# Kernel tuning notes

Measured on AMD Instinct MI355X. Metric: run time of the kernel, lower is better.

## Reference

```python
import jax, jax.numpy as jnp
import numpy as np
from jax import lax

_CLIP_MIN = 1e-06
_CLIP_MAX = 1.0
_POS_ALPHA = 0.0005
NUM_CLASSES = 21
RADIUS = 3
HALF_D = RADIUS * RADIUS
POOL = 3
PAD = POOL // 2
IGNORE = 255
LAM = 0.5  # loss_weight_lambda, lambda_way=1


def _max_pool(x):
    # NCHW max pool, kernel=stride=3, padding=1
    return lax.reduce_window(x, -jnp.inf, lax.max,
                             (1, 1, POOL, POOL), (1, 1, POOL, POOL),
                             ((0, 0), (0, 0), (PAD, PAD), (PAD, PAD)))


def _get_pairs(x):
    # stack radius*radius shifted crops -> [N, C, r^2, nh, nw]
    h, w = x.shape[2], x.shape[3]
    nh, nw = h - RADIUS + 1, w - RADIUS + 1
    crops = [x[:, :, y:y + nh, xo:xo + nw] for y in range(RADIUS) for xo in range(RADIUS)]
    return jnp.stack(crops, axis=2)


def _log_det_by_cholesky(m):
    chol = jnp.linalg.cholesky(m)
    return 2.0 * jnp.sum(jnp.log(jnp.diagonal(chol, axis1=-2, axis2=-1) + 1e-08), axis=-1)


def _rmi_lower_bound(labels_4d, probs_4d):
    la = _max_pool(labels_4d)
    pr = _max_pool(probs_4d)
    n, c = la.shape[0], la.shape[1]
    la_v = _get_pairs(la).reshape(n, c, HALF_D, -1)   # [N,C,d,L]
    pr_v = _get_pairs(pr).reshape(n, c, HALF_D, -1)
    la_v = la_v - jnp.mean(la_v, axis=3, keepdims=True)
    pr_v = pr_v - jnp.mean(pr_v, axis=3, keepdims=True)
    la_cov = jnp.einsum('ncdl,ncel->ncde', la_v, la_v)
    pr_cov = jnp.einsum('ncdl,ncel->ncde', pr_v, pr_v)
    eye = jnp.eye(HALF_D, dtype=la_cov.dtype)
    pr_cov_inv = jnp.linalg.inv(pr_cov + eye * _POS_ALPHA)
    la_pr_cov = jnp.einsum('ncdl,ncel->ncde', la_v, pr_v)
    appro_var = la_cov - jnp.einsum('ncde,ncef,ncgf->ncdg', la_pr_cov, pr_cov_inv, la_pr_cov)
    rmi_now = 0.5 * _log_det_by_cholesky(appro_var + eye * _POS_ALPHA)  # [N,C]
    rmi_per_class = jnp.mean(rmi_now.reshape(-1, NUM_CLASSES), axis=0) / float(HALF_D)
    return jnp.sum(rmi_per_class)


def setup_inputs() -> dict:
    key = jax.random.key(0)
    k1, k2 = jax.random.split(key)
    score = jax.random.normal(k1, (4, NUM_CLASSES, 512, 512), dtype=jnp.float32)
    target = jax.random.randint(k2, (4, 512, 512), 0, NUM_CLASSES, dtype=jnp.int64)
    return {"score": score, "target": target}


def reference(score, target):
    # cross entropy with ignore_index=255, mean reduction
    logp = jax.nn.log_softmax(score, axis=1)                      # [N,C,H,W]
    valid_ce = (target != IGNORE)
    safe_t = jnp.where(valid_ce, target, 0)
    nll = -jnp.take_along_axis(logp, safe_t[:, None].astype(jnp.int32), axis=1)[:, 0]
    normal_loss = jnp.sum(jnp.where(valid_ce, nll, 0.0)) / jnp.sum(valid_ce.astype(jnp.float32))

    # valid one-hot labels and masked sigmoid probs
    mask = (target < NUM_CLASSES)                                 # [N,H,W]
    maskf = mask.astype(jnp.float32)
    onehot = jax.nn.one_hot((target * mask).astype(jnp.int32), NUM_CLASSES, dtype=jnp.float32)
    onehot = onehot * maskf[..., None]                            # [N,H,W,C]
    onehot = jnp.transpose(onehot, (0, 3, 1, 2))                  # [N,C,H,W]
    probs = jnp.clip(jax.nn.sigmoid(score) * maskf[:, None], _CLIP_MIN, _CLIP_MAX)

    rmi_loss = _rmi_lower_bound(onehot, probs)
    return LAM * normal_loss + rmi_loss * (1.0 - LAM)
```

## Files before the change

### kernel.cpp

```cpp
#include <hip/hip_runtime.h>
#include <cfloat>
#include <cmath>

#define DEVINL __device__ __forceinline__

constexpr int N_ = 4, C_ = 21, H_ = 512, W_ = 512;
constexpr int P_ = 171;
constexpr int Q_ = 169;
constexpr int NC_ = N_ * C_;
constexpr int HW_ = H_ * W_;
constexpr int PP_ = 29241;
constexpr int PROW_ = 172;
constexpr int PPAD_ = PROW_ * P_;
constexpr int NCOV_ = 189;
constexpr float EPS_ = 5e-4f;
constexpr int RC_ = 29;
constexpr int G_ = 43;

DEVINL constexpr int tstart(int d) { return d * 9 - d * (d - 1) / 2; }

DEVINL float wave_sum(float v) {
#pragma unroll
    for (int o = 32; o > 0; o >>= 1) v += __shfl_down(v, o, 64);
    return v;
}

__global__ __launch_bounds__(256) void k_bits(const int* __restrict__ target,
                                              unsigned* __restrict__ pack) {
    int tid = blockIdx.x * 256 + threadIdx.x;
    if (tid >= N_ * PP_) return;
    int cell = tid % PP_;
    int n = tid / PP_;
    int j = cell % P_;
    int i = cell / P_;
    int hl = 3 * i - 1; if (hl < 0) hl = 0;
    int wl = 3 * j - 1; if (wl < 0) wl = 0;
    int hmax = 3 * i + 1, wmax = 3 * j + 1;
    const int* tb = target + (size_t)n * HW_;
    unsigned oh = 0, px = 0;
#pragma unroll
    for (int r = 0; r < 3; ++r) {
        int hh = hl + r;
        bool hv = hh <= hmax;
        const int* trow = tb + hh * W_;
#pragma unroll
        for (int dc = 0; dc < 3; ++dc) {
            int ww = wl + dc;
            int t = trow[ww];
            if (hv && (ww <= wmax) && t >= 0 && t < C_) {
                oh |= 1u << t;
                px |= 1u << (r * 3 + dc);
            }
        }
    }
    pack[tid] = oh | (px << 23);
}

__global__ __launch_bounds__(256) void k_ce(const float* __restrict__ score,
                                            const int* __restrict__ target,
                                            float* __restrict__ cov_ce) {
    int tid = blockIdx.x * 256 + threadIdx.x;
    int p0 = tid * 4;
    int n = p0 >> 18;
    int hw = p0 & (HW_ - 1);
    const float* sp = score + (size_t)n * C_ * HW_ + hw;

    float4 s[C_];
#pragma unroll
    for (int c = 0; c < C_; ++c)
        s[c] = *(const float4*)(sp + (size_t)c * HW_);
    int4 t4 = *(const int4*)(target + p0);

    float4 se = {0.f, 0.f, 0.f, 0.f};
    float4 stgt = {0.f, 0.f, 0.f, 0.f};
#pragma unroll
    for (int c = 0; c < C_; ++c) {
        se.x += __expf(s[c].x);
        se.y += __expf(s[c].y);
        se.z += __expf(s[c].z);
        se.w += __expf(s[c].w);
        if (t4.x == c) stgt.x = s[c].x;
        if (t4.y == c) stgt.y = s[c].y;
        if (t4.z == c) stgt.z = s[c].z;
        if (t4.w == c) stgt.w = s[c].w;
    }
    float nll = 0.f, cnt = 0.f;
    if (t4.x != 255) { nll += __logf(se.x) - stgt.x; cnt += 1.f; }
    if (t4.y != 255) { nll += __logf(se.y) - stgt.y; cnt += 1.f; }
    if (t4.z != 255) { nll += __logf(se.z) - stgt.z; cnt += 1.f; }
    if (t4.w != 255) { nll += __logf(se.w) - stgt.w; cnt += 1.f; }

    nll = wave_sum(nll);
    cnt = wave_sum(cnt);
    __shared__ float rn[4], rc[4];
    int wv = threadIdx.x >> 6, lane = threadIdx.x & 63;
    if (lane == 0) { rn[wv] = nll; rc[wv] = cnt; }
    __syncthreads();
    if (threadIdx.x == 0) {
        atomicAdd(&cov_ce[NC_ * NCOV_ + 0], rn[0] + rn[1] + rn[2] + rn[3]);
        atomicAdd(&cov_ce[NC_ * NCOV_ + 1], rc[0] + rc[1] + rc[2] + rc[3]);
    }
}

template <int IDX>
DEVINL void do_cell(const float (&f)[3][16], unsigned pk, int c, float* prp, float* lap) {
    unsigned px = pk >> 23;
    float vm = -FLT_MAX;
#pragma unroll
    for (int r = 0; r < 3; ++r)
#pragma unroll
        for (int dc = 0; dc < 3; ++dc)
            vm = fmaxf(vm, ((px >> (r * 3 + dc)) & 1u) ? f[r][IDX + dc] : -FLT_MAX);
    float p = __builtin_amdgcn_rcpf(1.f + __expf(-vm));
    p = fminf(fmaxf(p, 1e-6f), 1.f);
    *prp = p;
    *lap = ((pk >> c) & 1u) ? 1.f : 0.f;
}

__global__ __launch_bounds__(256) void k_pool(const float* __restrict__ score,
                                              const unsigned* __restrict__ pack,
                                              float* __restrict__ pr,
                                              float* __restrict__ la) {
    int tid = blockIdx.x * 256 + threadIdx.x;
    if (tid >= NC_ * P_ * G_) return;
    int g = tid % G_;
    int rest = tid / G_;
    int i = rest % P_;
    int ncidx = rest / P_;
    int n = ncidx / C_;
    int c = ncidx - n * C_;

    int hl = 3 * i - 1; if (hl < 0) hl = 0;
    int b = (g == 0) ? 0 : 12 * g - 4;
    int o3 = (b + 15 < W_) ? 12 : 8;

    const float* sb = score + (size_t)ncidx * HW_ + (size_t)hl * W_ + b;
    float f[3][16];
#pragma unroll
    for (int r = 0; r < 3; ++r) {
        const float* rp = sb + r * W_;
        float4 q0 = *(const float4*)(rp);
        float4 q1 = *(const float4*)(rp + 4);
        float4 q2 = *(const float4*)(rp + 8);
        float4 q3 = *(const float4*)(rp + o3);
        f[r][0] = q0.x;  f[r][1] = q0.y;  f[r][2] = q0.z;  f[r][3] = q0.w;
        f[r][4] = q1.x;  f[r][5] = q1.y;  f[r][6] = q1.z;  f[r][7] = q1.w;
        f[r][8] = q2.x;  f[r][9] = q2.y;  f[r][10] = q2.z; f[r][11] = q2.w;
        f[r][12] = q3.x; f[r][13] = q3.y; f[r][14] = q3.z; f[r][15] = q3.w;
    }

    const unsigned* pkp = pack + n * PP_ + i * P_ + 4 * g;
    size_t ob = (size_t)ncidx * PPAD_ + (size_t)i * PROW_ + 4 * g;
    if (g == 0) {
        do_cell<0>(f, pkp[0], c, pr + ob + 0, la + ob + 0);
        do_cell<2>(f, pkp[1], c, pr + ob + 1, la + ob + 1);
        do_cell<5>(f, pkp[2], c, pr + ob + 2, la + ob + 2);
        do_cell<8>(f, pkp[3], c, pr + ob + 3, la + ob + 3);
    } else {
        do_cell<3>(f, pkp[0], c, pr + ob + 0, la + ob + 0);
        do_cell<6>(f, pkp[1], c, pr + ob + 1, la + ob + 1);
        do_cell<9>(f, pkp[2], c, pr + ob + 2, la + ob + 2);
        if (4 * g + 3 < P_)
            do_cell<12>(f, pkp[3], c, pr + ob + 3, la + ob + 3);
    }
}

template <bool WITH_S1, int D0, int D1>
DEVINL void cov_tri(const float* __restrict__ X, float* __restrict__ cov,
                    int nc, int r0, int rend, int s1base, int s2base,
                    int tid, float (*red)[33]) {
    constexpr int NS2 = ((9 - D0) * (10 - D0) - (9 - D1) * (10 - D1)) / 2;
    constexpr int RLO = D0 / 3;
    constexpr int NS1 = WITH_S1 ? 9 : 0;
    constexpr int KOFF = tstart(D0);
    float s1[9], s2[NS2];
#pragma unroll
    for (int k = 0; k < 9; ++k) s1[k] = 0.f;
#pragma unroll
    for (int k = 0; k < NS2; ++k) s2[k] = 0.f;

    int nitems = (rend - r0) * G_;
    for (int idx = tid; idx < nitems; idx += 256) {
        int lr = idx / G_;
        int q = idx - lr * G_;
        int x0 = q * 4;
        const float* base = X + (size_t)(r0 + lr) * PROW_ + x0;
        float v[3][8];
#pragma unroll
        for (int r = RLO; r < 3; ++r) {
            float4 u0 = *(const float4*)(base + r * PROW_);
            float4 u1 = *(const float4*)(base + r * PROW_ + 4);
            v[r][0] = u0.x; v[r][1] = u0.y; v[r][2] = u0.z; v[r][3] = u0.w;
            v[r][4] = u1.x; v[r][5] = u1.y; v[r][6] = u1.z; v[r][7] = u1.w;
        }
#pragma unroll
        for (int p = 0; p < 4; ++p) {
            if (x0 + p < Q_) {
                if constexpr (WITH_S1) {
#pragma unroll
                    for (int d = 0; d < 9; ++d) s1[d] += v[d / 3][p + d % 3];
                }
                int k = 0;
#pragma unroll
                for (int d = D0; d < D1; ++d)
#pragma unroll
                    for (int e = d; e < 9; ++e) {
                        s2[k] += v[d / 3][p + d % 3] * v[e / 3][p + e % 3];
                        ++k;
                    }
            }
        }
    }

    int lane = tid & 63, wv = tid >> 6;
    if constexpr (WITH_S1) {
#pragma unroll
        for (int k = 0; k < 9; ++k) { float v2 = wave_sum(s1[k]); if (lane == 0) red[wv][k] = v2; }
    }
#pragma unroll
    for (int k = 0; k < NS2; ++k) { float v2 = wave_sum(s2[k]); if (lane == 0) red[wv][NS1 + k] = v2; }
    __syncthreads();
    for (int k = tid; k < NS1 + NS2; k += 256) {
        float v2 = red[0][k] + red[1][k] + red[2][k] + red[3][k];
        int dst = (WITH_S1 && k < 9) ? (s1base + k) : (s2base + KOFF + k - NS1);
        atomicAdd(&cov[nc * NCOV_ + dst], v2);
    }
}

template <int RA>
DEVINL void cov_ab(const float* __restrict__ A, const float* __restrict__ B,
                   float* __restrict__ cov, int nc, int r0, int rend,
                   int tid, float (*red)[33]) {
    float sab[27];
#pragma unroll
    for (int k = 0; k < 27; ++k) sab[k] = 0.f;

    int nitems = (rend - r0) * G_;
    for (int idx = tid; idx < nitems; idx += 256) {
        int lr = idx / G_;
        int q = idx - lr * G_;
        int x0 = q * 4;
        size_t off = (size_t)(r0 + lr) * PROW_ + x0;
        float a[8], b[3][8];
        {
            float4 u0 = *(const float4*)(A + off + RA * PROW_);
            float4 u1 = *(const float4*)(A + off + RA * PROW_ + 4);
            a[0] = u0.x; a[1] = u0.y; a[2] = u0.z; a[3] = u0.w;
            a[4] = u1.x; a[5] = u1.y; a[6] = u1.z; a[7] = u1.w;
        }
#pragma unroll
        for (int r = 0; r < 3; ++r) {
            float4 w0 = *(const float4*)(B + off + r * PROW_);
            float4 w1 = *(const float4*)(B + off + r * PROW_ + 4);
            b[r][0] = w0.x; b[r][1] = w0.y; b[r][2] = w0.z; b[r][3] = w0.w;
            b[r][4] = w1.x; b[r][5] = w1.y; b[r][6] = w1.z; b[r][7] = w1.w;
        }
#pragma unroll
        for (int p = 0; p < 4; ++p) {
            if (x0 + p < Q_) {
#pragma unroll
                for (int dm = 0; dm < 3; ++dm)
#pragma unroll
                    for (int e = 0; e < 9; ++e)
                        sab[dm * 9 + e] += a[p + dm] * b[e / 3][p + e % 3];
            }
        }
    }

    int lane = tid & 63, wv = tid >> 6;
#pragma unroll
    for (int k = 0; k < 27; ++k) { float v2 = wave_sum(sab[k]); if (lane == 0) red[wv][k] = v2; }
    __syncthreads();
    for (int k = tid; k < 27; k += 256) {
        float v2 = red[0][k] + red[1][k] + red[2][k] + red[3][k];
        atomicAdd(&cov[nc * NCOV_ + 108 + RA * 27 + k], v2);
    }
}

__global__ __launch_bounds__(256) void k_cov(const float* __restrict__ la,
                                             const float* __restrict__ pr,
                                             float* __restrict__ cov) {
    __shared__ float red[4][33];
    int nc = blockIdx.x;
    int chunk = blockIdx.y;
    int part = blockIdx.z;
    int r0 = chunk * RC_;
    int rend = r0 + RC_;
    if (rend > Q_) rend = Q_;
    int tid = threadIdx.x;
    const float* LA = la + (size_t)nc * PPAD_;
    const float* PR = pr + (size_t)nc * PPAD_;

    switch (part) {
        case 0: cov_tri<true, 0, 3>(LA, cov, nc, r0, rend, 0, 18, tid, red); break;
        case 1: cov_tri<false, 3, 9>(LA, cov, nc, r0, rend, 0, 18, tid, red); break;
        case 2: cov_tri<true, 0, 3>(PR, cov, nc, r0, rend, 9, 63, tid, red); break;
        case 3: cov_tri<false, 3, 9>(PR, cov, nc, r0, rend, 9, 63, tid, red); break;
        case 4: cov_ab<0>(LA, PR, cov, nc, r0, rend, tid, red); break;
        case 5: cov_ab<1>(LA, PR, cov, nc, r0, rend, tid, red); break;
        case 6: cov_ab<2>(LA, PR, cov, nc, r0, rend, tid, red); break;
    }
}

__global__ __launch_bounds__(128) void k_final(const float* __restrict__ cov,
                                               float* __restrict__ out) {
    __shared__ float red[128];
    int t = threadIdx.x;
    float my = 0.f;
    if (t < NC_) {
        const float* S = cov + t * NCOV_;
        const float Lf = (float)(Q_ * Q_);
        float sA[9], sB[9];
#pragma unroll
        for (int d = 0; d < 9; ++d) { sA[d] = S[d]; sB[d] = S[9 + d]; }
        float laC[45], M[45], Cm[81];
        {
            int k = 0;
#pragma unroll
            for (int d = 0; d < 9; ++d)
#pragma unroll
                for (int e = d; e < 9; ++e) {
                    laC[k] = S[18 + k] - sA[d] * sA[e] / Lf;
                    M[k] = S[63 + k] - sB[d] * sB[e] / Lf + (d == e ? EPS_ : 0.f);
                    ++k;
                }
#pragma unroll
            for (int d = 0; d < 9; ++d)
#pragma unroll
                for (int e = 0; e < 9; ++e)
                    Cm[d * 9 + e] = S[108 + d * 9 + e] - sA[d] * sB[e] / Lf;
        }
#pragma unroll
        for (int j = 0; j < 9; ++j) {
            float s = M[tstart(j)];
#pragma unroll
            for (int k = 0; k < j; ++k) { float l = M[tstart(k) + (j - k)]; s -= l * l; }
            float dj = sqrtf(fmaxf(s, 1e-30f));
            M[tstart(j)] = dj;
            float inv = 1.f / dj;
#pragma unroll
            for (int i = j + 1; i < 9; ++i) {
                float s2 = M[tstart(j) + (i - j)];
#pragma unroll
                for (int k = 0; k < j; ++k)
                    s2 -= M[tstart(k) + (i - k)] * M[tstart(k) + (j - k)];
                M[tstart(j) + (i - j)] = s2 * inv;
            }
        }
#pragma unroll
        for (int p = 0; p < 9; ++p) {
#pragma unroll
            for (int i = 0; i < 9; ++i) {
                float s = Cm[p * 9 + i];
#pragma unroll
                for (int k = 0; k < i; ++k)
                    s -= M[tstart(k) + (i - k)] * Cm[p * 9 + k];
                Cm[p * 9 + i] = s / M[tstart(i)];
            }
        }
#pragma unroll
        for (int d = 0; d < 9; ++d)
#pragma unroll
            for (int e = d; e < 9; ++e) {
                float s = 0.f;
#pragma unroll
                for (int i = 0; i < 9; ++i) s += Cm[d * 9 + i] * Cm[e * 9 + i];
                laC[tstart(d) + (e - d)] -= s;
                if (d == e) laC[tstart(d)] += EPS_;
            }
        float rmi = 0.f;
#pragma unroll
        for (int j = 0; j < 9; ++j) {
            float s = laC[tstart(j)];
#pragma unroll
            for (int k = 0; k < j; ++k) { float l = laC[tstart(k) + (j - k)]; s -= l * l; }
            float dj = sqrtf(fmaxf(s, 0.f));
            laC[tstart(j)] = dj;
            float inv = 1.f / fmaxf(dj, 1e-30f);
#pragma unroll
            for (int i = j + 1; i < 9; ++i) {
                float s2 = laC[tstart(j) + (i - j)];
#pragma unroll
                for (int k = 0; k < j; ++k)
                    s2 -= laC[tstart(k) + (i - k)] * laC[tstart(k) + (j - k)];
                laC[tstart(j) + (i - j)] = s2 * inv;
            }
            rmi += __logf(dj + 1e-8f);
        }
        my = rmi;
    }
    red[t] = my;
    __syncthreads();
#pragma unroll
    for (int o = 64; o > 0; o >>= 1) {
        if (t < o) red[t] += red[t + o];
        __syncthreads();
    }
    if (t == 0) {
        float rmi_total = red[0] / 36.f;
        float ce = cov[NC_ * NCOV_ + 0] / cov[NC_ * NCOV_ + 1];
        out[0] = 0.5f * ce + 0.5f * rmi_total;
    }
}

extern "C" void kernel_launch(void* const* d_in, const int* in_sizes, int n_in,
                              void* d_out, int out_size, void* d_ws, size_t ws_size,
                              hipStream_t stream) {
    const float* score = (const float*)d_in[0];
    const int* target = (const int*)d_in[1];
    float* pr = (float*)d_ws;
    float* la = pr + (size_t)NC_ * PPAD_;
    float* cov = la + (size_t)NC_ * PPAD_;
    unsigned* pack = (unsigned*)(cov + NC_ * NCOV_ + 2);
    hipMemsetAsync(cov, 0, (size_t)(NC_ * NCOV_ + 2) * sizeof(float), stream);

    k_bits<<<dim3((N_ * PP_ + 255) / 256), dim3(256), 0, stream>>>(target, pack);
    k_ce<<<dim3(N_ * HW_ / 4 / 256), dim3(256), 0, stream>>>(score, target, cov);
    k_pool<<<dim3((NC_ * P_ * G_ + 255) / 256), dim3(256), 0, stream>>>(score, pack, pr, la);
    k_cov<<<dim3(NC_, 6, 7), dim3(256), 0, stream>>>(la, pr, cov);
    k_final<<<dim3(1), dim3(128), 0, stream>>>(cov, (float*)d_out);
}
```

Before: 248.2 us.

## Fuse label packing, cross-entropy and max-pool into one row-band kernel

Merges the three preprocessing kernels (label bit packing, cross-entropy, pooled sigmoid) into a single kernel where each block handles one pooled row band of one image half. Score rows read for cross-entropy are meant to be reused from cache for the pooling pass, removing a second full read of score and the global pack buffer round trip plus two launches. Tradeoffs: only 1368 blocks, and the pooling loop uses scalar strided loads instead of vectorized float4 loads. The pooling writes are strided across classes, which may coalesce worse.

```diff
diff --git a/kernel.cpp b/kernel.cpp
--- a/kernel.cpp
+++ b/kernel.cpp
@@ -9,7 +9,6 @@
 constexpr int Q_ = 169;
 constexpr int NC_ = N_ * C_;
 constexpr int HW_ = H_ * W_;
-constexpr int PP_ = 29241;
 constexpr int PROW_ = 172;
 constexpr int PPAD_ = PROW_ * P_;
 constexpr int NCOV_ = 189;
@@ -25,143 +24,118 @@
     return v;
 }
 
-__global__ __launch_bounds__(256) void k_bits(const int* __restrict__ target,
-                                              unsigned* __restrict__ pack) {
-    int tid = blockIdx.x * 256 + threadIdx.x;
-    if (tid >= N_ * PP_) return;
-    int cell = tid % PP_;
-    int n = tid / PP_;
-    int j = cell % P_;
-    int i = cell / P_;
-    int hl = 3 * i - 1; if (hl < 0) hl = 0;
-    int wl = 3 * j - 1; if (wl < 0) wl = 0;
-    int hmax = 3 * i + 1, wmax = 3 * j + 1;
-    const int* tb = target + (size_t)n * HW_;
-    unsigned oh = 0, px = 0;
-#pragma unroll
-    for (int r = 0; r < 3; ++r) {
-        int hh = hl + r;
-        bool hv = hh <= hmax;
-        const int* trow = tb + hh * W_;
-#pragma unroll
-        for (int dc = 0; dc < 3; ++dc) {
-            int ww = wl + dc;
-            int t = trow[ww];
-            if (hv && (ww <= wmax) && t >= 0 && t < C_) {
-                oh |= 1u << t;
-                px |= 1u << (r * 3 + dc);
-            }
-        }
-    }
-    pack[tid] = oh | (px << 23);
-}
-
-__global__ __launch_bounds__(256) void k_ce(const float* __restrict__ score,
-                                            const int* __restrict__ target,
-                                            float* __restrict__ cov_ce) {
-    int tid = blockIdx.x * 256 + threadIdx.x;
-    int p0 = tid * 4;
-    int n = p0 >> 18;
-    int hw = p0 & (HW_ - 1);
-    const float* sp = score + (size_t)n * C_ * HW_ + hw;
-
-    float4 s[C_];
-#pragma unroll
-    for (int c = 0; c < C_; ++c)
-        s[c] = *(const float4*)(sp + (size_t)c * HW_);
-    int4 t4 = *(const int4*)(target + p0);
-
-    float4 se = {0.f, 0.f, 0.f, 0.f};
-    float4 stgt = {0.f, 0.f, 0.f, 0.f};
-#pragma unroll
-    for (int c = 0; c < C_; ++c) {
-        se.x += __expf(s[c].x);
-        se.y += __expf(s[c].y);
-        se.z += __expf(s[c].z);
-        se.w += __expf(s[c].w);
-        if (t4.x == c) stgt.x = s[c].x;
-        if (t4.y == c) stgt.y = s[c].y;
-        if (t4.z == c) stgt.z = s[c].z;
-        if (t4.w == c) stgt.w = s[c].w;
-    }
+__global__ __launch_bounds__(256) void k_fused(const float* __restrict__ score,
+                                               const int* __restrict__ target,
+                                               float* __restrict__ pr,
+                                               float* __restrict__ la,
+                                               float* __restrict__ cov) {
+    __shared__ unsigned sh_pack[86];
+    __shared__ float rn[4], rc[4];
+    int half = blockIdx.x;
+    int i = blockIdx.y;
+    int n = blockIdx.z;
+    int t = threadIdx.x;
+    int c0 = half * 256;
+    int jlo = half * 86;
+    int ncell = half ? 85 : 86;
+
     float nll = 0.f, cnt = 0.f;
-    if (t4.x != 255) { nll += __logf(se.x) - stgt.x; cnt += 1.f; }
-    if (t4.y != 255) { nll += __logf(se.y) - stgt.y; cnt += 1.f; }
-    if (t4.z != 255) { nll += __logf(se.z) - stgt.z; cnt += 1.f; }
-    if (t4.w != 255) { nll += __logf(se.w) - stgt.w; cnt += 1.f; }
-
+    {
+        int r = t >> 6, q = t & 63;
+        int rowbase = (i == 0) ? 0 : 3 * i - 1;
+        int nrows = (i == 0) ? 2 : 3;
+        if (r < nrows) {
+            int row = rowbase + r;
+            size_t pixoff = (size_t)row * W_ + c0 + 4 * q;
+            const float* sp = score + (size_t)n * C_ * HW_ + pixoff;
+            float4 s[C_];
+#pragma unroll
+            for (int c = 0; c < C_; ++c)
+                s[c] = *(const float4*)(sp + (size_t)c * HW_);
+            int4 t4 = *(const int4*)(target + (size_t)n * HW_ + pixoff);
+
+            float4 se = {0.f, 0.f, 0.f, 0.f};
+            float4 stgt = {0.f, 0.f, 0.f, 0.f};
+#pragma unroll
+            for (int c = 0; c < C_; ++c) {
+                se.x += __expf(s[c].x);
+                se.y += __expf(s[c].y);
+                se.z += __expf(s[c].z);
+                se.w += __expf(s[c].w);
+                if (t4.x == c) stgt.x = s[c].x;
+                if (t4.y == c) stgt.y = s[c].y;
+                if (t4.z == c) stgt.z = s[c].z;
+                if (t4.w == c) stgt.w = s[c].w;
+            }
+            if (t4.x != 255) { nll += __logf(se.x) - stgt.x; cnt += 1.f; }
+            if (t4.y != 255) { nll += __logf(se.y) - stgt.y; cnt += 1.f; }
+            if (t4.z != 255) { nll += __logf(se.z) - stgt.z; cnt += 1.f; }
+            if (t4.w != 255) { nll += __logf(se.w) - stgt.w; cnt += 1.f; }
+        }
+    }
     nll = wave_sum(nll);
     cnt = wave_sum(cnt);
-    __shared__ float rn[4], rc[4];
-    int wv = threadIdx.x >> 6, lane = threadIdx.x & 63;
-    if (lane == 0) { rn[wv] = nll; rc[wv] = cnt; }
+    {
+        int wv = t >> 6, lane = t & 63;
+        if (lane == 0) { rn[wv] = nll; rc[wv] = cnt; }
+    }
+
+    if (t < ncell) {
+        int j = jlo + t;
+        int hl = 3 * i - 1; if (hl < 0) hl = 0;
+        int wl = 3 * j - 1; if (wl < 0) wl = 0;
+        int hmax = 3 * i + 1, wmax = 3 * j + 1;
+        const int* tb = target + (size_t)n * HW_;
+        unsigned oh = 0, px = 0;
+#pragma unroll
+        for (int r = 0; r < 3; ++r) {
+            int hh = hl + r;
+            bool hv = hh <= hmax;
+            const int* trow = tb + hh * W_;
+#pragma unroll
+            for (int dc = 0; dc < 3; ++dc) {
+                int ww = wl + dc;
+                int tv = trow[ww];
+                if (hv && (ww <= wmax) && tv >= 0 && tv < C_) {
+                    oh |= 1u << tv;
+                    px |= 1u << (r * 3 + dc);
+                }
+            }
+        }
+        sh_pack[t] = oh | (px << 23);
+    }
     __syncthreads();
-    if (threadIdx.x == 0) {
-        atomicAdd(&cov_ce[NC_ * NCOV_ + 0], rn[0] + rn[1] + rn[2] + rn[3]);
-        atomicAdd(&cov_ce[NC_ * NCOV_ + 1], rc[0] + rc[1] + rc[2] + rc[3]);
-    }
-}
-
-template <int IDX>
-DEVINL void do_cell(const float (&f)[3][16], unsigned pk, int c, float* prp, float* lap) {
-    unsigned px = pk >> 23;
-    float vm = -FLT_MAX;
-#pragma unroll
-    for (int r = 0; r < 3; ++r)
-#pragma unroll
-        for (int dc = 0; dc < 3; ++dc)
-            vm = fmaxf(vm, ((px >> (r * 3 + dc)) & 1u) ? f[r][IDX + dc] : -FLT_MAX);
-    float p = __builtin_amdgcn_rcpf(1.f + __expf(-vm));
-    p = fminf(fmaxf(p, 1e-6f), 1.f);
-    *prp = p;
-    *lap = ((pk >> c) & 1u) ? 1.f : 0.f;
-}
-
-__global__ __launch_bounds__(256) void k_pool(const float* __restrict__ score,
-                                              const unsigned* __restrict__ pack,
-                                              float* __restrict__ pr,
-                                              float* __restrict__ la) {
-    int tid = blockIdx.x * 256 + threadIdx.x;
-    if (tid >= NC_ * P_ * G_) return;
-    int g = tid % G_;
-    int rest = tid / G_;
-    int i = rest % P_;
-    int ncidx = rest / P_;
-    int n = ncidx / C_;
-    int c = ncidx - n * C_;
+
+    if (t == 0)
+        atomicAdd(&cov[NC_ * NCOV_ + 0], rn[0] + rn[1] + rn[2] + rn[3]);
+    if (t == 64)
+        atomicAdd(&cov[NC_ * NCOV_ + 1], rc[0] + rc[1] + rc[2] + rc[3]);
 
     int hl = 3 * i - 1; if (hl < 0) hl = 0;
-    int b = (g == 0) ? 0 : 12 * g - 4;
-    int o3 = (b + 15 < W_) ? 12 : 8;
-
-    const float* sb = score + (size_t)ncidx * HW_ + (size_t)hl * W_ + b;
-    float f[3][16];
-#pragma unroll
-    for (int r = 0; r < 3; ++r) {
-        const float* rp = sb + r * W_;
-        float4 q0 = *(const float4*)(rp);
-        float4 q1 = *(const float4*)(rp + 4);
-        float4 q2 = *(const float4*)(rp + 8);
-        float4 q3 = *(const float4*)(rp + o3);
-        f[r][0] = q0.x;  f[r][1] = q0.y;  f[r][2] = q0.z;  f[r][3] = q0.w;
-        f[r][4] = q1.x;  f[r][5] = q1.y;  f[r][6] = q1.z;  f[r][7] = q1.w;
-        f[r][8] = q2.x;  f[r][9] = q2.y;  f[r][10] = q2.z; f[r][11] = q2.w;
-        f[r][12] = q3.x; f[r][13] = q3.y; f[r][14] = q3.z; f[r][15] = q3.w;
-    }
-
-    const unsigned* pkp = pack + n * PP_ + i * P_ + 4 * g;
-    size_t ob = (size_t)ncidx * PPAD_ + (size_t)i * PROW_ + 4 * g;
-    if (g == 0) {
-        do_cell<0>(f, pkp[0], c, pr + ob + 0, la + ob + 0);
-        do_cell<2>(f, pkp[1], c, pr + ob + 1, la + ob + 1);
-        do_cell<5>(f, pkp[2], c, pr + ob + 2, la + ob + 2);
-        do_cell<8>(f, pkp[3], c, pr + ob + 3, la + ob + 3);
-    } else {
-        do_cell<3>(f, pkp[0], c, pr + ob + 0, la + ob + 0);
-        do_cell<6>(f, pkp[1], c, pr + ob + 1, la + ob + 1);
-        do_cell<9>(f, pkp[2], c, pr + ob + 2, la + ob + 2);
-        if (4 * g + 3 < P_)
-            do_cell<12>(f, pkp[3], c, pr + ob + 3, la + ob + 3);
+    for (int item = t; item < C_ * 86; item += 256) {
+        int c = item / 86;
+        int jj = item - c * 86;
+        if (jj >= ncell) continue;
+        int j = jlo + jj;
+        int wl = 3 * j - 1; if (wl < 0) wl = 0;
+        int ncidx = n * C_ + c;
+        const float* sp = score + (size_t)ncidx * HW_ + (size_t)hl * W_ + wl;
+        unsigned pk = sh_pack[jj];
+        unsigned px = pk >> 23;
+        float vm = -FLT_MAX;
+#pragma unroll
+        for (int r = 0; r < 3; ++r) {
+#pragma unroll
+            for (int dc = 0; dc < 3; ++dc) {
+                float v = sp[r * W_ + dc];
+                vm = fmaxf(vm, ((px >> (r * 3 + dc)) & 1u) ? v : -FLT_MAX);
+            }
+        }
+        float p = __builtin_amdgcn_rcpf(1.f + __expf(-vm));
+        p = fminf(fmaxf(p, 1e-6f), 1.f);
+        size_t ob = (size_t)ncidx * PPAD_ + (size_t)i * PROW_ + j;
+        pr[ob] = p;
+        la[ob] = ((pk >> c) & 1u) ? 1.f : 0.f;
     }
 }
 
@@ -411,12 +385,9 @@
     float* pr = (float*)d_ws;
     float* la = pr + (size_t)NC_ * PPAD_;
     float* cov = la + (size_t)NC_ * PPAD_;
-    unsigned* pack = (unsigned*)(cov + NC_ * NCOV_ + 2);
     hipMemsetAsync(cov, 0, (size_t)(NC_ * NCOV_ + 2) * sizeof(float), stream);
 
-    k_bits<<<dim3((N_ * PP_ + 255) / 256), dim3(256), 0, stream>>>(target, pack);
-    k_ce<<<dim3(N_ * HW_ / 4 / 256), dim3(256), 0, stream>>>(score, target, cov);
-    k_pool<<<dim3((NC_ * P_ * G_ + 255) / 256), dim3(256), 0, stream>>>(score, pack, pr, la);
+    k_fused<<<dim3(2, P_, N_), dim3(256), 0, stream>>>(score, target, pr, la, cov);
     k_cov<<<dim3(NC_, 6, 7), dim3(256), 0, stream>>>(la, pr, cov);
     k_final<<<dim3(1), dim3(128), 0, stream>>>(cov, (float*)d_out);
 }
```

Result: no change. 246.6 us (-0.7%).
